# Optimization experiments

Hardware: AMD Instinct MI355X
Metric: run time of the kernel (lower is better)

The kernel has to match this reference:

```python
import jax, jax.numpy as jnp
import numpy as np

B, CIN, COUT, K, H, W = 8, 512, 512, 3, 64, 64
SCALE = 1.0 / np.sqrt(CIN * K * K).astype(np.float32)  # conv.scale
LRELU_SCALE = 1.4142135623730951  # sqrt(2), FusedLeakyReLU scale


def setup_inputs() -> dict:
    key = jax.random.key(0)
    ks = jax.random.split(key, 6)
    return {
        "x": jax.random.normal(ks[0], (B, CIN, H, W), jnp.float32),
        "style": jax.random.normal(ks[1], (B, CIN), jnp.float32),
        "noise": jax.random.normal(ks[2], (1, 1, H, W), jnp.float32),
        "weight": jax.random.normal(ks[3], (COUT, CIN, K, K), jnp.float32),
        "bias": jnp.zeros((COUT,), jnp.float32),
        "noise_strength": jax.random.uniform(ks[4], (1,), jnp.float32),
    }


def reference(x, style, noise, weight, bias, noise_strength):
    # Modulate: scale * weight * style  -> [B, Cout, Cin, K, K]
    w = SCALE * weight[None] * style[:, None, :, None, None]
    # Demodulate per (batch, out_channel)
    demod = jax.lax.rsqrt(jnp.sum(w * w, axis=(2, 3, 4)) + 1e-8)
    w = w * demod[:, :, None, None, None]
    # Per-sample conv (grouped-conv trick in torch) via vmap over batch
    pad = K // 2
    def conv_one(xi, wi):  # xi: [Cin,H,W], wi: [Cout,Cin,K,K]
        return jax.lax.conv_general_dilated(
            xi[None], wi, window_strides=(1, 1),
            padding=[(pad, pad), (pad, pad)],
            dimension_numbers=("NCHW", "OIHW", "NCHW"))[0]
    out = jax.vmap(conv_one)(x, w)  # [B, Cout, H, W]
    # NoiseInjection: out + strength * noise (noise broadcast over B, C)
    out = out + noise_strength[0] * noise
    # FusedLeakyReLU: leaky_relu(out + bias, 0.2) * sqrt(2)
    y = out + bias[None, :, None, None]
    return jnp.where(y >= 0, y, 0.2 * y) * LRELU_SCALE
```

## Files before the change

kernel.cpp:

```cpp
#include <hip/hip_runtime.h>
#include <hip/hip_bf16.h>

typedef __attribute__((ext_vector_type(8))) short s16x8;
typedef __attribute__((ext_vector_type(16))) float f32x16;

#define MOD_SCALE 0.014731391274719739f

__device__ __forceinline__ void gload_lds16(const void* g, void* l) {
    __builtin_amdgcn_global_load_lds(
        (const __attribute__((address_space(1))) unsigned int*)g,
        (__attribute__((address_space(3))) unsigned int*)l, 16, 0, 0);
}

__device__ __forceinline__ void sync_drain() {
    __builtin_amdgcn_s_waitcnt(0);
    __syncthreads();
}

__global__ __launch_bounds__(256) void k_prep(const float* __restrict__ x,
                                              const float* __restrict__ style,
                                              const float* __restrict__ weight,
                                              __hip_bfloat16* __restrict__ xs,
                                              __hip_bfloat16* __restrict__ wb,
                                              float* __restrict__ dem) {
    __shared__ __align__(16) char sm[16896];
    const int t = threadIdx.x;
    const int bid = blockIdx.x;

    if (bid < 520) {
        const int idx = bid * 256 + t;
        const int b = idx / 16640;
        const int r2 = idx - b * 16640;
        const int pair = r2 >> 6;
        const int ciq = r2 & 63;
        int pr, pc;
        if (pair < 66)       { pr = 0;          pc = pair; }
        else if (pair < 132) { pr = 65;         pc = pair - 66; }
        else if (pair < 196) { pr = pair - 131; pc = 0; }
        else                 { pr = pair - 195; pc = 65; }
        uint4* d = (uint4*)(xs + (((size_t)b * 66 + pr) * 66 + pc) * 512) + ciq;
        *d = make_uint4(0u, 0u, 0u, 0u);
    } else if (bid < 2568) {
        const int r = bid - 520;
        const int cig = r & 3, h = (r >> 2) & 63, b = r >> 8;
        const int ci0 = cig * 128;
        __hip_bfloat16 (*tile)[130] = (__hip_bfloat16(*)[130])sm;
        const int wl = t & 63, cl4 = t >> 6;
        for (int rr = 0; rr < 32; ++rr) {
            int c = rr * 4 + cl4;
            float v = x[(((size_t)b * 512 + ci0 + c) * 64 + h) * 64 + wl];
            float s = style[b * 512 + ci0 + c];
            tile[wl][c] = __float2bfloat16(v * s * MOD_SCALE);
        }
        __syncthreads();
        const int w4 = t >> 6;
        const int cp = (t & 63) * 2;
        for (int rr = 0; rr < 16; ++rr) {
            int w = rr * 4 + w4;
            unsigned v = *(const unsigned*)(&tile[w][cp]);
            *(unsigned*)(&xs[(((size_t)b * 66 + h + 1) * 66 + (w + 1)) * 512 +
                             ci0 + cp]) = v;
        }
    } else if (bid < 3592) {
        const int r = bid - 2568;
        float* lds = (float*)sm;
        const int p0 = r * 256;
        const float* src = weight + (size_t)p0 * 9;
#pragma unroll
        for (int k = 0; k < 9; ++k) lds[k * 256 + t] = src[k * 256 + t];
        __syncthreads();
#pragma unroll
        for (int tap = 0; tap < 9; ++tap)
            wb[(size_t)tap * 262144 + p0 + t] = __float2bfloat16(lds[t * 9 + tap]);
    } else {
        const int co = bid - 3592;
        float* s2 = (float*)sm;
        for (int i = t; i < 4096; i += 256) { float v = style[i]; s2[i] = v * v; }
        __syncthreads();
        const float4* wp = (const float4*)(weight + (size_t)co * 4608);
        float acc[8] = {0.f, 0.f, 0.f, 0.f, 0.f, 0.f, 0.f, 0.f};
        for (int j = t; j < 1152; j += 256) {
            float4 v = wp[j];
            float w2[4] = {v.x * v.x, v.y * v.y, v.z * v.z, v.w * v.w};
            int base = j * 4;
#pragma unroll
            for (int e = 0; e < 4; ++e) {
                int ci = (base + e) / 9;
                float ww = w2[e];
#pragma unroll
                for (int bb = 0; bb < 8; ++bb) acc[bb] += ww * s2[bb * 512 + ci];
            }
        }
#pragma unroll
        for (int bb = 0; bb < 8; ++bb)
            for (int off = 32; off > 0; off >>= 1)
                acc[bb] += __shfl_down(acc[bb], off);
        float* red = (float*)(sm + 16384);
        const int wv = t >> 6, lane = t & 63;
        if (lane == 0) {
#pragma unroll
            for (int bb = 0; bb < 8; ++bb) red[wv * 8 + bb] = acc[bb];
        }
        __syncthreads();
        if (t < 8) {
            float s = red[t] + red[8 + t] + red[16 + t] + red[24 + t];
            const float S2 = MOD_SCALE * MOD_SCALE;
            dem[t * 512 + co] = rsqrtf(S2 * s + 1e-8f);
        }
    }
}

__global__ __launch_bounds__(256, 2) void k_conv(
    const __hip_bfloat16* __restrict__ xs,
    const __hip_bfloat16* __restrict__ wb,
    const float* __restrict__ demod,
    const float* __restrict__ noise,
    const float* __restrict__ bias,
    const float* __restrict__ nstr,
    float* __restrict__ out) {
    __shared__ __align__(16) char Xl[25344];
    __shared__ __align__(16) char Wl[6][8192];

    const int t = threadIdx.x;
    const int bi = blockIdx.x;
    const int spat = bi & 127;
    const int b = spat >> 4;
    const int h0 = (spat & 15) << 2;
    const int co0 = (bi >> 7) << 7;
    const int lane = t & 63;
    const int wv = t >> 6;
    const int wm = wv & 1, wn = wv >> 1;
    const int el = lane & 31;
    const int hk = lane >> 5;

    f32x16 acc[2][4];
#pragma unroll
    for (int i = 0; i < 2; ++i)
#pragma unroll
        for (int j = 0; j < 4; ++j)
#pragma unroll
            for (int k = 0; k < 16; ++k) acc[i][j][k] = 0.f;

    const char* xsb = (const char*)xs + (size_t)b * 66 * 66 * 1024;
    const char* xsrc[7];
#pragma unroll
    for (int i = 0; i < 6; ++i) {
        int g = i * 256 + t;
        int e = g >> 2, s = g & 3;
        int gc = (s - (e >> 2)) & 3;
        int row = e / 66, col = e - row * 66;
        xsrc[i] = xsb + (size_t)((h0 + row) * 66 + col) * 1024 + gc * 16;
    }
    {
        int g = 1536 + t;
        int e = g >> 2, s = g & 3;
        int gc = (s - (e >> 2)) & 3;
        int row = e / 66, col = e - row * 66;
        xsrc[6] = xsb + (size_t)((h0 + row) * 66 + col) * 1024 + gc * 16;
    }
    const char* wsrc[2];
#pragma unroll
    for (int i = 0; i < 2; ++i) {
        int g = i * 256 + t;
        int e = g >> 2, s = g & 3;
        int gc = (s - (e >> 2)) & 3;
        wsrc[i] = (const char*)wb + (size_t)(co0 + e) * 1024 + gc * 16;
    }
    const int wvoff = wv << 10;

#pragma unroll
    for (int i = 0; i < 6; ++i) gload_lds16(xsrc[i], Xl + i * 4096 + wvoff);
    if (t < 48) gload_lds16(xsrc[6], Xl + 24576);
#pragma unroll
    for (int tt = 0; tt < 3; ++tt)
#pragma unroll
        for (int i = 0; i < 2; ++i)
            gload_lds16(wsrc[i] + (size_t)tt * 524288,
                        Wl[tt] + i * 4096 + wvoff);
    sync_drain();

    int cboff = 0;
    for (int cb = 0; cb < 16; ++cb, cboff += 64) {
        const int ncboff = (cb < 15) ? cboff + 64 : cboff;
#pragma unroll
        for (int p = 0; p < 3; ++p) {
            const int bank = ((cb + p) & 1) * 3;
            const int nbank = 3 - bank;
#pragma unroll
            for (int tt = 0; tt < 3; ++tt) {
                const size_t soff = (p < 2)
                    ? (size_t)(3 * (p + 1) + tt) * 524288 + cboff
                    : (size_t)tt * 524288 + ncboff;
                char* dst = Wl[nbank + tt] + wvoff;
#pragma unroll
                for (int i = 0; i < 2; ++i)
                    gload_lds16(wsrc[i] + soff, dst + i * 4096);
            }
#pragma unroll
            for (int tt = 0; tt < 3; ++tt) {
                const char* Wb = Wl[bank + tt];
#pragma unroll
                for (int ks = 0; ks < 2; ++ks) {
                    const int c = 2 * ks + hk;
                    s16x8 af[2], bfr[4];
#pragma unroll
                    for (int mi = 0; mi < 2; ++mi) {
                        int e = wm * 64 + mi * 32 + el;
                        af[mi] = *(const s16x8*)(Wb + e * 64 +
                                                 (((c + (e >> 2)) & 3) << 4));
                    }
#pragma unroll
                    for (int ni = 0; ni < 4; ++ni) {
                        int e = (2 * wn + (ni >> 1) + p) * 66 + tt +
                                (ni & 1) * 32 + el;
                        bfr[ni] = *(const s16x8*)(Xl + e * 64 +
                                                  (((c + (e >> 2)) & 3) << 4));
                    }
#pragma unroll
                    for (int mi = 0; mi < 2; ++mi)
#pragma unroll
                        for (int ni = 0; ni < 4; ++ni)
                            acc[mi][ni] =
                                __builtin_amdgcn_mfma_f32_32x32x16_bf16(
                                    af[mi], bfr[ni], acc[mi][ni], 0, 0, 0);
                }
            }
            sync_drain();
        }
        if (cb < 15) {
#pragma unroll
            for (int i = 0; i < 6; ++i)
                gload_lds16(xsrc[i] + cboff + 64, Xl + i * 4096 + wvoff);
            if (t < 48) gload_lds16(xsrc[6] + cboff + 64, Xl + 24576);
            sync_drain();
        }
    }

    const float nsv = nstr[0];
    const float LR = 1.4142135623730951f;
#pragma unroll
    for (int mi = 0; mi < 2; ++mi) {
        float dm[16], bs[16];
#pragma unroll
        for (int rg = 0; rg < 16; ++rg) {
            int co = co0 + wm * 64 + mi * 32 + (rg & 3) + 8 * (rg >> 2) + 4 * hk;
            dm[rg] = demod[b * 512 + co];
            bs[rg] = bias[co];
        }
#pragma unroll
        for (int ni = 0; ni < 4; ++ni) {
            int h = h0 + 2 * wn + (ni >> 1);
            int w = (ni & 1) * 32 + el;
            float nz = nsv * noise[h * 64 + w];
#pragma unroll
            for (int rg = 0; rg < 16; ++rg) {
                int co = co0 + wm * 64 + mi * 32 + (rg & 3) + 8 * (rg >> 2) +
                         4 * hk;
                float v = acc[mi][ni][rg] * dm[rg] + nz + bs[rg];
                v = (v >= 0.f ? v : 0.2f * v) * LR;
                out[(((size_t)b * 512 + co) * 64 + h) * 64 + w] = v;
            }
        }
    }
}

extern "C" void kernel_launch(void* const* d_in, const int* in_sizes, int n_in,
                              void* d_out, int out_size, void* d_ws, size_t ws_size,
                              hipStream_t stream) {
    const float* x      = (const float*)d_in[0];
    const float* style  = (const float*)d_in[1];
    const float* noise  = (const float*)d_in[2];
    const float* weight = (const float*)d_in[3];
    const float* bias   = (const float*)d_in[4];
    const float* nstr   = (const float*)d_in[5];
    float* out = (float*)d_out;

    char* ws = (char*)d_ws;
    __hip_bfloat16* xs = (__hip_bfloat16*)ws;
    __hip_bfloat16* wb = (__hip_bfloat16*)(ws + 35684352);
    float* demod = (float*)(ws + 35684352 + 4718592);

    k_prep<<<4104, 256, 0, stream>>>(x, style, weight, xs, wb, demod);
    k_conv<<<512, 256, 0, stream>>>(xs, wb, demod, noise, bias, nstr, out);
}
```

Before: 256.0 us.

## Block activation staging by 32-channel groups and widen prep transpose tiles

Changes the padded bf16 activation buffer from a channels-last layout (512 channels per pixel) to 16 channel-blocks of 32 channels, each holding a full padded image. The conv kernel's per-iteration loads then touch contiguous 64-byte pixel rows within one block instead of striding across 1 KB pixels. The prep transpose now handles a whole row across all 512 channels per block with float4 reads and 16-byte writes, so it needs fewer blocks. This costs a much larger LDS allocation in the prep kernel, which lowers its occupancy.

```diff
diff --git a/kernel.cpp b/kernel.cpp
--- a/kernel.cpp
+++ b/kernel.cpp
@@ -23,7 +23,7 @@
                                               __hip_bfloat16* __restrict__ xs,
                                               __hip_bfloat16* __restrict__ wb,
                                               float* __restrict__ dem) {
-    __shared__ __align__(16) char sm[16896];
+    __shared__ __align__(16) char sm[71680];
     const int t = threadIdx.x;
     const int bid = blockIdx.x;
 
@@ -31,38 +31,55 @@
         const int idx = bid * 256 + t;
         const int b = idx / 16640;
         const int r2 = idx - b * 16640;
-        const int pair = r2 >> 6;
-        const int ciq = r2 & 63;
+        const int cb = r2 / 1040;
+        const int r3 = r2 - cb * 1040;
+        const int pair = r3 >> 2;
+        const int chunk = r3 & 3;
         int pr, pc;
         if (pair < 66)       { pr = 0;          pc = pair; }
         else if (pair < 132) { pr = 65;         pc = pair - 66; }
         else if (pair < 196) { pr = pair - 131; pc = 0; }
         else                 { pr = pair - 195; pc = 65; }
-        uint4* d = (uint4*)(xs + (((size_t)b * 66 + pr) * 66 + pc) * 512) + ciq;
-        *d = make_uint4(0u, 0u, 0u, 0u);
-    } else if (bid < 2568) {
+        char* d = (char*)xs +
+                  ((size_t)(b * 16 + cb) * 4356 + pr * 66 + pc) * 64 +
+                  chunk * 16;
+        *(uint4*)d = make_uint4(0u, 0u, 0u, 0u);
+    } else if (bid < 1032) {
         const int r = bid - 520;
-        const int cig = r & 3, h = (r >> 2) & 63, b = r >> 8;
-        const int ci0 = cig * 128;
-        __hip_bfloat16 (*tile)[130] = (__hip_bfloat16(*)[130])sm;
-        const int wl = t & 63, cl4 = t >> 6;
-        for (int rr = 0; rr < 32; ++rr) {
-            int c = rr * 4 + cl4;
-            float v = x[(((size_t)b * 512 + ci0 + c) * 64 + h) * 64 + wl];
-            float s = style[b * 512 + ci0 + c];
-            tile[wl][c] = __float2bfloat16(v * s * MOD_SCALE);
-        }
-        __syncthreads();
-        const int w4 = t >> 6;
-        const int cp = (t & 63) * 2;
-        for (int rr = 0; rr < 16; ++rr) {
-            int w = rr * 4 + w4;
-            unsigned v = *(const unsigned*)(&tile[w][cp]);
-            *(unsigned*)(&xs[(((size_t)b * 66 + h + 1) * 66 + (w + 1)) * 512 +
-                             ci0 + cp]) = v;
-        }
-    } else if (bid < 3592) {
-        const int r = bid - 2568;
+        const int b = r >> 6, h = r & 63;
+        __hip_bfloat16 (*tile)[68] = (__hip_bfloat16(*)[68])sm;
+        float* sf = (float*)(sm + 69632);
+        sf[t] = style[b * 512 + t] * MOD_SCALE;
+        sf[t + 256] = style[b * 512 + 256 + t] * MOD_SCALE;
+        __syncthreads();
+        const float* xb = x + (size_t)b * 512 * 4096 + h * 64;
+#pragma unroll 4
+        for (int it = 0; it < 32; ++it) {
+            int idx = it * 256 + t;
+            int ci = idx >> 4, w4 = idx & 15;
+            float4 v = *(const float4*)(xb + (size_t)ci * 4096 + w4 * 4);
+            float s = sf[ci];
+            union { uint2 u2; __hip_bfloat16 q[4]; } pk;
+            pk.q[0] = __float2bfloat16(v.x * s);
+            pk.q[1] = __float2bfloat16(v.y * s);
+            pk.q[2] = __float2bfloat16(v.z * s);
+            pk.q[3] = __float2bfloat16(v.w * s);
+            *(uint2*)&tile[ci][w4 * 4] = pk.u2;
+        }
+        __syncthreads();
+        const int cig = t & 3, w = t >> 2;
+        char* ob = (char*)xs + (size_t)b * 4460544 +
+                   (size_t)((h + 1) * 66 + 1) * 64;
+#pragma unroll
+        for (int cb = 0; cb < 16; ++cb) {
+            union { uint4 u; __hip_bfloat16 q[8]; } pk;
+#pragma unroll
+            for (int j = 0; j < 8; ++j)
+                pk.q[j] = tile[cb * 32 + cig * 8 + j][w];
+            *(uint4*)(ob + (size_t)cb * 278784 + w * 64 + cig * 16) = pk.u;
+        }
+    } else if (bid < 2056) {
+        const int r = bid - 1032;
         float* lds = (float*)sm;
         const int p0 = r * 256;
         const float* src = weight + (size_t)p0 * 9;
@@ -73,7 +90,7 @@
         for (int tap = 0; tap < 9; ++tap)
             wb[(size_t)tap * 262144 + p0 + t] = __float2bfloat16(lds[t * 9 + tap]);
     } else {
-        const int co = bid - 3592;
+        const int co = bid - 2056;
         float* s2 = (float*)sm;
         for (int i = t; i < 4096; i += 256) { float v = style[i]; s2[i] = v * v; }
         __syncthreads();
@@ -141,7 +158,7 @@
 #pragma unroll
             for (int k = 0; k < 16; ++k) acc[i][j][k] = 0.f;
 
-    const char* xsb = (const char*)xs + (size_t)b * 66 * 66 * 1024;
+    const char* xsb = (const char*)xs + (size_t)b * 4460544;
     const char* xsrc[7];
 #pragma unroll
     for (int i = 0; i < 6; ++i) {
@@ -149,14 +166,14 @@
         int e = g >> 2, s = g & 3;
         int gc = (s - (e >> 2)) & 3;
         int row = e / 66, col = e - row * 66;
-        xsrc[i] = xsb + (size_t)((h0 + row) * 66 + col) * 1024 + gc * 16;
+        xsrc[i] = xsb + (size_t)((h0 + row) * 66 + col) * 64 + gc * 16;
     }
     {
         int g = 1536 + t;
         int e = g >> 2, s = g & 3;
         int gc = (s - (e >> 2)) & 3;
         int row = e / 66, col = e - row * 66;
-        xsrc[6] = xsb + (size_t)((h0 + row) * 66 + col) * 1024 + gc * 16;
+        xsrc[6] = xsb + (size_t)((h0 + row) * 66 + col) * 64 + gc * 16;
     }
     const char* wsrc[2];
 #pragma unroll
@@ -228,10 +245,11 @@
             sync_drain();
         }
         if (cb < 15) {
+            const size_t xo = (size_t)(cb + 1) * 278784;
 #pragma unroll
             for (int i = 0; i < 6; ++i)
-                gload_lds16(xsrc[i] + cboff + 64, Xl + i * 4096 + wvoff);
-            if (t < 48) gload_lds16(xsrc[6] + cboff + 64, Xl + 24576);
+                gload_lds16(xsrc[i] + xo, Xl + i * 4096 + wvoff);
+            if (t < 48) gload_lds16(xsrc[6] + xo, Xl + 24576);
             sync_drain();
         }
     }
@@ -280,6 +298,6 @@
     __hip_bfloat16* wb = (__hip_bfloat16*)(ws + 35684352);
     float* demod = (float*)(ws + 35684352 + 4718592);
 
-    k_prep<<<4104, 256, 0, stream>>>(x, style, weight, xs, wb, demod);
+    k_prep<<<2568, 256, 0, stream>>>(x, style, weight, xs, wb, demod);
     k_conv<<<512, 256, 0, stream>>>(xs, wb, demod, noise, bias, nstr, out);
 }
```

Result: no change. 252.6 us (-1.3%).
